# Optimization experiments

Hardware: AMD Instinct MI355X
Metric: run time of the kernel (lower is better)

Reference implementation:

```python
import jax, jax.numpy as jnp
import numpy as np

N = 50000      # num_nodes
E = 800000     # num_edges
D_IN = 128
D_HID = 128
D_EMB = 128
G = 4          # num_gcns
BN_EPS = 1e-5


def setup_inputs() -> dict:
    key = jax.random.key(0)
    ks = jax.random.split(key, 8)
    x = jax.random.normal(ks[0], (N, D_IN), dtype=jnp.float32)
    edge_index = jax.random.randint(ks[1], (2, E), 0, N, dtype=jnp.int64)
    # per-GCN params, stacked on leading G axis
    W1 = jax.random.normal(ks[2], (G, D_IN, D_HID), dtype=jnp.float32) / np.sqrt(D_IN)
    b1 = jnp.zeros((G, D_HID), dtype=jnp.float32)
    W2 = jax.random.normal(ks[3], (G, D_HID, D_EMB), dtype=jnp.float32) / np.sqrt(D_HID)
    b2 = jnp.zeros((G, D_EMB), dtype=jnp.float32)
    gamma1 = jnp.ones((G, D_HID), dtype=jnp.float32)
    beta1 = jnp.zeros((G, D_HID), dtype=jnp.float32)
    gamma2 = jnp.ones((G, D_EMB), dtype=jnp.float32)
    beta2 = jnp.zeros((G, D_EMB), dtype=jnp.float32)
    alpha = jnp.asarray(0.25, dtype=jnp.float32)  # PReLU (single shared param)
    mix_embed = jnp.full((N, G), 1.0 / G, dtype=jnp.float32)
    return {"x": x, "edge_index": edge_index, "W1": W1, "b1": b1, "W2": W2,
            "b2": b2, "gamma1": gamma1, "beta1": beta1, "gamma2": gamma2,
            "beta2": beta2, "alpha": alpha, "mix_embed": mix_embed}


def _gcn_norm(edge_index, num_nodes):
    # PyG GCNConv: add self-loops, symmetric normalization D^-1/2 (A+I) D^-1/2
    row, col = edge_index[0], edge_index[1]
    loop = jnp.arange(num_nodes, dtype=edge_index.dtype)
    row = jnp.concatenate([row, loop])
    col = jnp.concatenate([col, loop])
    w = jnp.ones(row.shape[0], dtype=jnp.float32)
    deg = jax.ops.segment_sum(w, col, num_segments=num_nodes)
    dinv = jnp.where(deg > 0, deg ** -0.5, 0.0)
    norm = dinv[row] * w * dinv[col]
    return row, col, norm


def _propagate(h, row, col, norm, num_nodes):
    # gather from source, scale by edge norm, scatter-add to target
    msg = h[row] * norm[:, None]
    return jax.ops.segment_sum(msg, col, num_segments=num_nodes)


def _batchnorm(z, gamma, beta):
    mu = jnp.mean(z, axis=0)
    var = jnp.mean((z - mu) ** 2, axis=0)  # biased, as torch BN training mode
    return (z - mu) * jax.lax.rsqrt(var + BN_EPS) * gamma + beta


def _prelu(z, alpha):
    return jnp.where(z > 0, z, alpha * z)


def reference(x, edge_index, W1, b1, W2, b2, gamma1, beta1, gamma2, beta2, alpha, mix_embed):
    num_nodes = x.shape[0]
    row, col, norm = _gcn_norm(edge_index, num_nodes)
    mix = jax.nn.softmax(mix_embed, axis=-1)  # [N, G]
    out = jnp.zeros((num_nodes, D_EMB), dtype=x.dtype)
    for g in range(G):  # small fixed number of mixture components
        h = x @ W1[g]
        z = _propagate(h, row, col, norm, num_nodes) + b1[g]
        z = _prelu(_batchnorm(z, gamma1[g], beta1[g]), alpha)
        h = z @ W2[g]
        z = _propagate(h, row, col, norm, num_nodes) + b2[g]
        z = _prelu(_batchnorm(z, gamma2[g], beta2[g]), alpha)
        out = out + mix[:, g:g + 1] * z
    return out
```

## Files before the change

### kernel.cpp

```cpp
#include <hip/hip_runtime.h>
#include <stdint.h>

static constexpr float EPS = 1e-5f;
static constexpr int XB = 64;

typedef __attribute__((ext_vector_type(8))) short bfrag;
typedef __attribute__((ext_vector_type(4))) float ffrag;

__device__ __forceinline__ float bf2f(unsigned short u){
  union { unsigned int i; float f; } v; v.i = ((unsigned int)u) << 16; return v.f;
}
__device__ __forceinline__ unsigned short f2bf(float f){
  union { float f; unsigned int i; } v; v.f = f;
  unsigned int x = v.i;
  x += 0x7fffu + ((x >> 16) & 1u);
  return (unsigned short)(x >> 16);
}
__device__ __forceinline__ float lo16(unsigned int v){ return bf2f((unsigned short)(v & 0xffffu)); }
__device__ __forceinline__ float hi16(unsigned int v){ return bf2f((unsigned short)(v >> 16)); }
__device__ __forceinline__ unsigned int pack2(float a, float b){
  return ((unsigned int)f2bf(b) << 16) | (unsigned int)f2bf(a);
}

__global__ __launch_bounds__(256) void k_deg(const int* __restrict__ col, int* __restrict__ indeg,
                                             int N, int E, int dbl,
                                             const float* __restrict__ W1, const float* __restrict__ W2,
                                             unsigned short* __restrict__ Wt1, unsigned short* __restrict__ Wt2){
  int b = blockIdx.x;
  if (b < dbl){
    int e0 = (b * 256 + threadIdx.x) * 2;
    if (e0 < E){
      if (e0 + 1 < E){
        int2 cc = *(const int2*)&col[e0];
        unsigned c0 = (unsigned)cc.x, c1 = (unsigned)cc.y;
        if (c0 < (unsigned)N) atomicAdd(&indeg[c0], 1);
        if (c1 < (unsigned)N) atomicAdd(&indeg[c1], 1);
      } else {
        unsigned c0 = (unsigned)col[e0];
        if (c0 < (unsigned)N) atomicAdd(&indeg[c0], 1);
      }
    }
  } else {
    int idx = (b - dbl) * 256 + threadIdx.x;
    const float* W = W1; unsigned short* Wt = Wt1;
    if (idx >= 65536){ idx -= 65536; W = W2; Wt = Wt2; }
    int c = idx >> 7, k = idx & 127;
    int g = c >> 7, j = c & 127;
    Wt[(size_t)c * 128 + k] = f2bf(W[(size_t)g*16384 + k*128 + j]);
  }
}

__global__ void k_alloc(const int* __restrict__ indeg, int* __restrict__ ctr,
                        int* __restrict__ offs, int* __restrict__ cursor,
                        float* __restrict__ dinv, int N){
  int tid = blockIdx.x * 256 + threadIdx.x;
  int lane = threadIdx.x & 63;
  int v = (tid < N) ? indeg[tid] : 0;
  int incl = v;
  #pragma unroll
  for (int d = 1; d < 64; d <<= 1){
    int u = __shfl_up(incl, d);
    if (lane >= d) incl += u;
  }
  int base = 0;
  if (lane == 63) base = atomicAdd(ctr, incl);
  base = __shfl(base, 63);
  if (tid < N){
    int o = base + incl - v;
    offs[tid] = o; cursor[tid] = o;
    dinv[tid] = rsqrtf((float)(v + 1));
  }
}

__global__ __launch_bounds__(256) void k_scatter(const int* __restrict__ row, const int* __restrict__ col,
                                                 int* __restrict__ cursor, int* __restrict__ csr,
                                                 int N, int E, int sbl,
                                                 const float* __restrict__ x, const float* __restrict__ dinv,
                                                 unsigned short* __restrict__ xs, int total4x){
  int b = blockIdx.x;
  if (b < sbl){
    int e0 = (b * 256 + threadIdx.x) * 2;
    #pragma unroll
    for (int q = 0; q < 2; q++){
      int e = e0 + q;
      if (e < E){
        unsigned c = (unsigned)col[e];
        if (c < (unsigned)N){
          int p = atomicAdd(&cursor[c], 1);
          unsigned r = (unsigned)row[e];
          csr[p] = (r < (unsigned)N) ? (int)r : 0;
        }
      }
    }
  } else {
    int idx = (b - sbl) * 256 + threadIdx.x;
    int stride = (gridDim.x - sbl) * 256;
    for (; idx < total4x; idx += stride){
      int i = idx >> 5;
      float di = dinv[i];
      float4 v = ((const float4*)x)[idx];
      ushort4 o;
      o.x = f2bf(di * v.x); o.y = f2bf(di * v.y);
      o.z = f2bf(di * v.z); o.w = f2bf(di * v.w);
      ((ushort4*)xs)[idx] = o;
    }
  }
}

__global__ __launch_bounds__(256) void k_prop_x(const unsigned int* __restrict__ xs2,
                                               const int* __restrict__ csr,
                                               const int* __restrict__ offs, const int* __restrict__ indeg,
                                               const float* __restrict__ dinv,
                                               unsigned int* __restrict__ s2, int N){
  int i = blockIdx.x * 4 + (threadIdx.x >> 6);
  if (i >= N) return;
  int c2 = threadIdx.x & 63;
  unsigned int sv = xs2[(size_t)i*64 + c2];
  float ax = lo16(sv), ay = hi16(sv);
  int e = offs[i], end = e + indeg[i];
  for (; e + 8 <= end; e += 8){
    int r0 = csr[e], r1 = csr[e+1], r2 = csr[e+2], r3 = csr[e+3];
    int r4 = csr[e+4], r5 = csr[e+5], r6 = csr[e+6], r7 = csr[e+7];
    unsigned int v0 = xs2[(size_t)r0*64 + c2], v1 = xs2[(size_t)r1*64 + c2];
    unsigned int v2 = xs2[(size_t)r2*64 + c2], v3 = xs2[(size_t)r3*64 + c2];
    unsigned int v4 = xs2[(size_t)r4*64 + c2], v5 = xs2[(size_t)r5*64 + c2];
    unsigned int v6 = xs2[(size_t)r6*64 + c2], v7 = xs2[(size_t)r7*64 + c2];
    ax += lo16(v0)+lo16(v1)+lo16(v2)+lo16(v3)+lo16(v4)+lo16(v5)+lo16(v6)+lo16(v7);
    ay += hi16(v0)+hi16(v1)+hi16(v2)+hi16(v3)+hi16(v4)+hi16(v5)+hi16(v6)+hi16(v7);
  }
  for (; e < end; e++){
    unsigned int v = xs2[(size_t)csr[e]*64 + c2];
    ax += lo16(v); ay += hi16(v);
  }
  float di = dinv[i];
  s2[(size_t)i*64 + c2] = pack2(di * ax, di * ay);
}

__global__ __launch_bounds__(256) void k_gram(const unsigned short* __restrict__ in,
                                              int rstride, int coff128,
                                              float* __restrict__ Gpart, float* __restrict__ msumbase,
                                              int N){
  int gy = blockIdx.y;
  const unsigned short* src = in + gy * coff128;
  float* Gp = Gpart + ((size_t)gy * XB + blockIdx.x) * 16384;
  float* msum = msumbase + gy * 128;

  __shared__ unsigned short st[128 * 40];
  __shared__ float colsum[128];

  int t = threadIdx.x;
  int wv = t >> 6, lane = t & 63, l16 = lane & 15, quad = lane >> 4;
  if (t < 128) colsum[t] = 0.f;

  int sn = t & 31, scb = t >> 5;

  ffrag acc[2][8];
  #pragma unroll
  for (int a = 0; a < 2; a++)
    #pragma unroll
    for (int b = 0; b < 8; b++) acc[a][b] = (ffrag){0.f,0.f,0.f,0.f};

  float cs[16];
  #pragma unroll
  for (int j = 0; j < 16; j++) cs[j] = 0.f;

  for (int c0 = blockIdx.x * 32; c0 < N; c0 += gridDim.x * 32){
    __syncthreads();
    int n = c0 + sn;
    ushort4 u0, u1, u2, u3;
    if (n < N){
      const ushort4* p = (const ushort4*)(src + (size_t)n * rstride + scb * 16);
      u0 = p[0]; u1 = p[1]; u2 = p[2]; u3 = p[3];
    } else {
      u0 = u1 = u2 = u3 = (ushort4){0,0,0,0};
    }
    unsigned short vals[16] = {u0.x,u0.y,u0.z,u0.w, u1.x,u1.y,u1.z,u1.w,
                               u2.x,u2.y,u2.z,u2.w, u3.x,u3.y,u3.z,u3.w};
    #pragma unroll
    for (int j = 0; j < 16; j++){
      st[(scb * 16 + j) * 40 + sn] = vals[j];
      cs[j] += bf2f(vals[j]);
    }
    __syncthreads();
    #pragma unroll
    for (int ta = 0; ta < 2; ta++){
      int ra = wv * 2 + ta;
      bfrag af = *(const bfrag*)&st[(ra * 16 + l16) * 40 + quad * 8];
      #pragma unroll
      for (int tb = 0; tb < 8; tb++){
        bfrag bf = *(const bfrag*)&st[(tb * 16 + l16) * 40 + quad * 8];
        acc[ta][tb] = __builtin_amdgcn_mfma_f32_16x16x32_bf16(af, bf, acc[ta][tb], 0, 0, 0);
      }
    }
  }
  #pragma unroll
  for (int j = 0; j < 16; j++) atomicAdd(&colsum[scb * 16 + j], cs[j]);
  __syncthreads();
  if (t < 128) atomicAdd(&msum[t], colsum[t]);
  #pragma unroll
  for (int ta = 0; ta < 2; ta++){
    #pragma unroll
    for (int tb = 0; tb < 8; tb++){
      int row0 = wv * 32 + ta * 16 + quad * 4;
      int colg = tb * 16 + l16;
      #pragma unroll
      for (int r = 0; r < 4; r++)
        Gp[(size_t)(row0 + r) * 128 + colg] = acc[ta][tb][r];
    }
  }
}

__global__ __launch_bounds__(256) void k_gred(const float* __restrict__ Gpart, float* __restrict__ G){
  int i = blockIdx.x * 256 + threadIdx.x;
  int grp = blockIdx.y;
  const float* src = Gpart + (size_t)grp * XB * 16384;
  float s = 0.f;
  #pragma unroll 4
  for (int xb = 0; xb < XB; xb++) s += src[(size_t)xb * 16384 + i];
  G[(size_t)grp * 16384 + i] = s;
}

__global__ __launch_bounds__(64) void k_bnfit(const float* __restrict__ W,
                                              const float* __restrict__ gamma, const float* __restrict__ beta,
                                              const float* __restrict__ Gbase, int gmul,
                                              const float* __restrict__ msumbase, int mmul,
                                              float* __restrict__ scale, float* __restrict__ shiftF,
                                              float invN){
  int c = blockIdx.x;
  int g = c >> 7, j = c & 127;
  const float* Wc = W + (size_t)g * 16384 + j;
  const float* G  = Gbase + (size_t)g * gmul;
  const float* mv = msumbase + g * mmul;
  __shared__ float wl[128];
  __shared__ float ml[128];
  int t = threadIdx.x;
  for (int k = t; k < 128; k += 64){ wl[k] = Wc[(size_t)k * 128]; ml[k] = mv[k] * invN; }
  __syncthreads();
  float quad = 0.f, dm = 0.f;
  #pragma unroll
  for (int kk = 0; kk < 2; kk++){
    int k = t + kk * 64;
    float wk = wl[k];
    dm += ml[k] * wk;
    const float* Gr = G + (size_t)k * 128;
    float p = 0.f;
    for (int jj = 0; jj < 128; jj += 4){
      float4 gg = *(const float4*)(Gr + jj);
      float4 ww = *(const float4*)(wl + jj);
      p += gg.x*ww.x + gg.y*ww.y + gg.z*ww.z + gg.w*ww.w;
    }
    quad += wk * p;
  }
  for (int o = 32; o > 0; o >>= 1){
    quad += __shfl_down(quad, o);
    dm   += __shfl_down(dm, o);
  }
  if (t == 0){
    float var = quad * invN - dm * dm;
    float sc = gamma[c] * rsqrtf(var + EPS);
    scale[c] = sc;
    shiftF[c] = beta[c] - dm * sc;
  }
}

__global__ __launch_bounds__(256) void k_mm1f(const unsigned short* __restrict__ in,
                                              const unsigned short* __restrict__ Wt,
                                              const float* __restrict__ scale, const float* __restrict__ shiftF,
                                              const float* __restrict__ alpha_p, const float* __restrict__ dinv,
                                              unsigned short* __restrict__ h, int N){
  float alpha = alpha_p[0];
  int wave = threadIdx.x >> 6, lane = threadIdx.x & 63;
  int l16 = lane & 15, quad = lane >> 4;
  int node = blockIdx.x * 16 + l16;
  int nc = node < N ? node : N - 1;
  int colbase0 = wave * 128;
  float di = dinv[nc];

  const unsigned short* inrow = in + (size_t)nc * 128 + quad * 8;
  bfrag b0 = *(const bfrag*)(inrow);
  bfrag b1 = *(const bfrag*)(inrow + 32);
  bfrag b2 = *(const bfrag*)(inrow + 64);
  bfrag b3 = *(const bfrag*)(inrow + 96);

  #pragma unroll
  for (int ct = 0; ct < 8; ct++){
    int colbase = colbase0 + ct * 16;
    const unsigned short* wrow = Wt + (size_t)(colbase + l16) * 128 + quad * 8;
    bfrag a0 = *(const bfrag*)(wrow);
    bfrag a1 = *(const bfrag*)(wrow + 32);
    bfrag a2 = *(const bfrag*)(wrow + 64);
    bfrag a3 = *(const bfrag*)(wrow + 96);
    ffrag acc = {0.f, 0.f, 0.f, 0.f};
    acc = __builtin_amdgcn_mfma_f32_16x16x32_bf16(a0, b0, acc, 0, 0, 0);
    acc = __builtin_amdgcn_mfma_f32_16x16x32_bf16(a1, b1, acc, 0, 0, 0);
    acc = __builtin_amdgcn_mfma_f32_16x16x32_bf16(a2, b2, acc, 0, 0, 0);
    acc = __builtin_amdgcn_mfma_f32_16x16x32_bf16(a3, b3, acc, 0, 0, 0);
    int cb = colbase + quad * 4;
    float4 sc = *(const float4*)(scale + cb);
    float4 sh = *(const float4*)(shiftF + cb);
    float v0 = acc[0]*sc.x + sh.x; v0 = v0 > 0.f ? v0 : alpha*v0;
    float v1 = acc[1]*sc.y + sh.y; v1 = v1 > 0.f ? v1 : alpha*v1;
    float v2 = acc[2]*sc.z + sh.z; v2 = v2 > 0.f ? v2 : alpha*v2;
    float v3 = acc[3]*sc.w + sh.w; v3 = v3 > 0.f ? v3 : alpha*v3;
    uint2 o;
    o.x = pack2(di*v0, di*v1);
    o.y = pack2(di*v2, di*v3);
    if (node < N)
      *(uint2*)(h + (size_t)node * 512 + cb) = o;
  }
}

__global__ __launch_bounds__(256) void k_prop_h(const unsigned int* __restrict__ h2,
                                                const int* __restrict__ csr,
                                                const int* __restrict__ offs, const int* __restrict__ indeg,
                                                const float* __restrict__ dinv,
                                                unsigned int* __restrict__ t2, int N){
  int B = blockIdx.x;
  int s = B & 3;
  int i = (B >> 2) * 4 + (threadIdx.x >> 6);
  if (i >= N) return;
  int c2 = s * 64 + (threadIdx.x & 63);
  unsigned int sv = h2[(size_t)i*256 + c2];
  float ax = lo16(sv), ay = hi16(sv);
  int e = offs[i], end = e + indeg[i];
  for (; e + 16 <= end; e += 16){
    int r[16];
    #pragma unroll
    for (int j = 0; j < 16; j++) r[j] = csr[e + j];
    unsigned int v[16];
    #pragma unroll
    for (int j = 0; j < 16; j++) v[j] = h2[(size_t)r[j]*256 + c2];
    #pragma unroll
    for (int j = 0; j < 16; j++){ ax += lo16(v[j]); ay += hi16(v[j]); }
  }
  for (; e + 4 <= end; e += 4){
    int r0 = csr[e], r1 = csr[e+1], r2 = csr[e+2], r3 = csr[e+3];
    unsigned int v0 = h2[(size_t)r0*256 + c2], v1 = h2[(size_t)r1*256 + c2];
    unsigned int v2 = h2[(size_t)r2*256 + c2], v3 = h2[(size_t)r3*256 + c2];
    ax += lo16(v0)+lo16(v1)+lo16(v2)+lo16(v3);
    ay += hi16(v0)+hi16(v1)+hi16(v2)+hi16(v3);
  }
  for (; e < end; e++){
    unsigned int v = h2[(size_t)csr[e]*256 + c2];
    ax += lo16(v); ay += hi16(v);
  }
  float di = dinv[i];
  t2[(size_t)i*256 + c2] = pack2(di * ax, di * ay);
}

__global__ __launch_bounds__(256) void k_mm2f(const unsigned short* __restrict__ t,
                                              const unsigned short* __restrict__ Wt,
                                              const float* __restrict__ scale, const float* __restrict__ shiftF,
                                              const float* __restrict__ alpha_p, const float* __restrict__ mixe,
                                              float* __restrict__ out, int N){
  __shared__ float red[4][16][132];
  float alpha = alpha_p[0];
  int wave = threadIdx.x >> 6, lane = threadIdx.x & 63;
  int l16 = lane & 15, quad = lane >> 4;
  int node = blockIdx.x * 16 + l16;
  int nc = node < N ? node : N - 1;

  float4 me = ((const float4*)mixe)[nc];
  float mx = fmaxf(fmaxf(me.x, me.y), fmaxf(me.z, me.w));
  float e0 = __expf(me.x - mx), e1 = __expf(me.y - mx), e2 = __expf(me.z - mx), e3 = __expf(me.w - mx);
  float inv = 1.f / (e0 + e1 + e2 + e3);
  float wvx = ((wave == 0) ? e0 : (wave == 1) ? e1 : (wave == 2) ? e2 : e3) * inv;

  const unsigned short* inrow = t + (size_t)nc * 512 + wave * 128 + quad * 8;
  bfrag b0 = *(const bfrag*)(inrow);
  bfrag b1 = *(const bfrag*)(inrow + 32);
  bfrag b2 = *(const bfrag*)(inrow + 64);
  bfrag b3 = *(const bfrag*)(inrow + 96);

  #pragma unroll
  for (int ct = 0; ct < 8; ct++){
    int c512 = wave * 128 + ct * 16;
    const unsigned short* wrow = Wt + (size_t)(c512 + l16) * 128 + quad * 8;
    bfrag a0 = *(const bfrag*)(wrow);
    bfrag a1 = *(const bfrag*)(wrow + 32);
    bfrag a2 = *(const bfrag*)(wrow + 64);
    bfrag a3 = *(const bfrag*)(wrow + 96);
    ffrag acc = {0.f, 0.f, 0.f, 0.f};
    acc = __builtin_amdgcn_mfma_f32_16x16x32_bf16(a0, b0, acc, 0, 0, 0);
    acc = __builtin_amdgcn_mfma_f32_16x16x32_bf16(a1, b1, acc, 0, 0, 0);
    acc = __builtin_amdgcn_mfma_f32_16x16x32_bf16(a2, b2, acc, 0, 0, 0);
    acc = __builtin_amdgcn_mfma_f32_16x16x32_bf16(a3, b3, acc, 0, 0, 0);
    int cb = c512 + quad * 4;
    float4 sc = *(const float4*)(scale + cb);
    float4 sh = *(const float4*)(shiftF + cb);
    float v0 = acc[0]*sc.x + sh.x; v0 = v0 > 0.f ? v0 : alpha*v0;
    float v1 = acc[1]*sc.y + sh.y; v1 = v1 > 0.f ? v1 : alpha*v1;
    float v2 = acc[2]*sc.z + sh.z; v2 = v2 > 0.f ? v2 : alpha*v2;
    float v3 = acc[3]*sc.w + sh.w; v3 = v3 > 0.f ? v3 : alpha*v3;
    int j = ct * 16 + quad * 4;
    float4 wr = {wvx*v0, wvx*v1, wvx*v2, wvx*v3};
    *(float4*)&red[wave][l16][j] = wr;
  }
  __syncthreads();
  int tt = threadIdx.x;
  int nn = tt >> 4, j0 = (tt & 15) * 8;
  int gnode = blockIdx.x * 16 + nn;
  if (gnode < N){
    float4 r0 = {0,0,0,0}, r1 = {0,0,0,0};
    #pragma unroll
    for (int w = 0; w < 4; w++){
      float4 p0 = *(const float4*)&red[w][nn][j0];
      float4 p1 = *(const float4*)&red[w][nn][j0 + 4];
      r0.x += p0.x; r0.y += p0.y; r0.z += p0.z; r0.w += p0.w;
      r1.x += p1.x; r1.y += p1.y; r1.z += p1.z; r1.w += p1.w;
    }
    float* op = out + (size_t)gnode * 128 + j0;
    *(float4*)(op) = r0;
    *(float4*)(op + 4) = r1;
  }
}

extern "C" void kernel_launch(void* const* d_in, const int* in_sizes, int n_in,
                              void* d_out, int out_size, void* d_ws, size_t ws_size,
                              hipStream_t stream) {
  const float* x      = (const float*)d_in[0];
  const int*   ei     = (const int*)d_in[1];
  const float* W1     = (const float*)d_in[2];
  const float* W2     = (const float*)d_in[4];
  const float* gamma1 = (const float*)d_in[6];
  const float* beta1  = (const float*)d_in[7];
  const float* gamma2 = (const float*)d_in[8];
  const float* beta2  = (const float*)d_in[9];
  const float* alpha  = (const float*)d_in[10];
  const float* mixe   = (const float*)d_in[11];
  float* out = (float*)d_out;

  const int N = in_sizes[0] / 128;
  const int E = in_sizes[1] / 2;
  const int* rowv = ei;
  const int* colv = ei + E;

  char* w = (char*)d_ws;
  size_t off = 0;
  auto take = [&](size_t bytes) -> void* {
    void* p = w + off;
    off = (off + bytes + 255) & ~(size_t)255;
    return p;
  };
  size_t zbeg = off;
  int*   indeg  = (int*)take((size_t)N * 4);
  int*   ctr    = (int*)take(256);
  float* m1     = (float*)take(512);
  float* m2     = (float*)take(2048);
  size_t zend = off;
  float* G1     = (float*)take(65536);
  float* G2     = (float*)take(262144);
  float* Gpart  = (float*)take((size_t)4 * XB * 16384 * 4);
  int*   cursor = (int*)take((size_t)N * 4);
  int*   offs   = (int*)take((size_t)N * 4);
  float* dinv   = (float*)take((size_t)N * 4);
  float* scale1 = (float*)take(2048);
  float* shift1 = (float*)take(2048);
  float* scale2 = (float*)take(2048);
  float* shift2 = (float*)take(2048);
  int*   csr    = (int*)take((size_t)E * 4);
  unsigned short* Wt1 = (unsigned short*)take(512 * 128 * 2);
  unsigned short* Wt2 = (unsigned short*)take(512 * 128 * 2);
  unsigned short* xs = (unsigned short*)take((size_t)N * 128 * 2);
  unsigned short* sb = (unsigned short*)take((size_t)N * 128 * 2);
  unsigned short* h  = (unsigned short*)take((size_t)N * 512 * 2);
  unsigned short* tb = (unsigned short*)take((size_t)N * 512 * 2);

  hipMemsetAsync((char*)d_ws + zbeg, 0, zend - zbeg, stream);

  int nb  = (N + 255) / 256;
  int dbl = (E + 511) / 512;
  float invN = 1.0f / (float)N;

  k_deg<<<dbl + 512, 256, 0, stream>>>(colv, indeg, N, E, dbl, W1, W2, Wt1, Wt2);
  k_alloc<<<nb, 256, 0, stream>>>(indeg, ctr, offs, cursor, dinv, N);
  k_scatter<<<dbl + 1024, 256, 0, stream>>>(rowv, colv, cursor, csr, N, E, dbl, x, dinv, xs, N * 32);

  k_prop_x<<<(N + 3) / 4, 256, 0, stream>>>((const unsigned int*)xs, csr, offs, indeg, dinv, (unsigned int*)sb, N);

  k_gram<<<dim3(XB, 1), 256, 0, stream>>>(sb, 128, 0, Gpart, m1, N);
  k_gred<<<dim3(64, 1), 256, 0, stream>>>(Gpart, G1);
  k_bnfit<<<512, 64, 0, stream>>>(W1, gamma1, beta1, G1, 0, m1, 0, scale1, shift1, invN);
  k_mm1f<<<(N + 15) / 16, 256, 0, stream>>>(sb, Wt1, scale1, shift1, alpha, dinv, h, N);

  k_prop_h<<<((N + 3) / 4) * 4, 256, 0, stream>>>((const unsigned int*)h, csr, offs, indeg, dinv, (unsigned int*)tb, N);

  k_gram<<<dim3(XB, 4), 256, 0, stream>>>(tb, 512, 128, Gpart, m2, N);
  k_gred<<<dim3(64, 4), 256, 0, stream>>>(Gpart, G2);
  k_bnfit<<<512, 64, 0, stream>>>(W2, gamma2, beta2, G2, 16384, m2, 128, scale2, shift2, invN);
  k_mm2f<<<(N + 15) / 16, 256, 0, stream>>>(tb, Wt2, scale2, shift2, alpha, mixe, out, N);
}
```

Baseline: 568.7 us.

## Fuse graph-build and BN-fit stages into persistent kernels with grid barriers

Merges degree counting, offset allocation and CSR scatter into one 512-block persistent kernel separated by atomic grid barriers. It also merges the Gram, reduction and BN-fit stages into a single kernel per layer. The goal is to cut launch count and inter-kernel gaps. Separately, it widens the k_prop_x gather unroll to 16 and makes k_mm1f handle 32 nodes per block so weight fragments are reused. The grid barriers assume every block is co-resident on the device, and spinning blocks plus less parallelism in the fused stages may cost time.

```diff
diff --git a/kernel.cpp b/kernel.cpp
--- a/kernel.cpp
+++ b/kernel.cpp
@@ -22,64 +22,73 @@
   return ((unsigned int)f2bf(b) << 16) | (unsigned int)f2bf(a);
 }
 
-__global__ __launch_bounds__(256) void k_deg(const int* __restrict__ col, int* __restrict__ indeg,
-                                             int N, int E, int dbl,
-                                             const float* __restrict__ W1, const float* __restrict__ W2,
-                                             unsigned short* __restrict__ Wt1, unsigned short* __restrict__ Wt2){
-  int b = blockIdx.x;
-  if (b < dbl){
-    int e0 = (b * 256 + threadIdx.x) * 2;
-    if (e0 < E){
-      if (e0 + 1 < E){
-        int2 cc = *(const int2*)&col[e0];
-        unsigned c0 = (unsigned)cc.x, c1 = (unsigned)cc.y;
-        if (c0 < (unsigned)N) atomicAdd(&indeg[c0], 1);
-        if (c1 < (unsigned)N) atomicAdd(&indeg[c1], 1);
-      } else {
-        unsigned c0 = (unsigned)col[e0];
-        if (c0 < (unsigned)N) atomicAdd(&indeg[c0], 1);
+__device__ __forceinline__ void gbar(int* cnt, int target){
+  __threadfence();
+  __syncthreads();
+  if (threadIdx.x == 0){
+    __hip_atomic_fetch_add(cnt, 1, __ATOMIC_ACQ_REL, __HIP_MEMORY_SCOPE_AGENT);
+    while (__hip_atomic_load(cnt, __ATOMIC_ACQUIRE, __HIP_MEMORY_SCOPE_AGENT) < target){
+      __builtin_amdgcn_s_sleep(8);
+    }
+  }
+  __syncthreads();
+}
+
+__global__ __launch_bounds__(256) void k_graph(const int* __restrict__ row, const int* __restrict__ col,
+                                               int N, int E,
+                                               int* __restrict__ indeg, int* __restrict__ ctr,
+                                               int* __restrict__ offs, int* __restrict__ cursor,
+                                               float* __restrict__ dinv, int* __restrict__ csr,
+                                               const float* __restrict__ x, unsigned short* __restrict__ xs,
+                                               const float* __restrict__ W1, const float* __restrict__ W2,
+                                               unsigned short* __restrict__ Wt1, unsigned short* __restrict__ Wt2,
+                                               int* __restrict__ bars){
+  int bid = blockIdx.x;
+  int gid = bid * 256 + threadIdx.x;
+  int gstride = gridDim.x * 256;
+  int target = gridDim.x;
+
+  for (int e0 = gid * 2; e0 < E; e0 += gstride * 2){
+    if (e0 + 1 < E){
+      int2 cc = *(const int2*)&col[e0];
+      unsigned c0 = (unsigned)cc.x, c1 = (unsigned)cc.y;
+      if (c0 < (unsigned)N) atomicAdd(&indeg[c0], 1);
+      if (c1 < (unsigned)N) atomicAdd(&indeg[c1], 1);
+    } else {
+      unsigned c0 = (unsigned)col[e0];
+      if (c0 < (unsigned)N) atomicAdd(&indeg[c0], 1);
+    }
+  }
+  for (int idx = gid; idx < 131072; idx += gstride){
+    int i2 = idx; const float* W = W1; unsigned short* Wt = Wt1;
+    if (i2 >= 65536){ i2 -= 65536; W = W2; Wt = Wt2; }
+    int c = i2 >> 7, k = i2 & 127;
+    Wt[(size_t)c * 128 + k] = f2bf(W[(size_t)(c >> 7) * 16384 + k * 128 + (c & 127)]);
+  }
+  gbar(&bars[0], target);
+
+  {
+    int wv = threadIdx.x >> 6, lane = threadIdx.x & 63;
+    int nwaves = gridDim.x * 4;
+    for (int wb = bid * 4 + wv; wb * 64 < N; wb += nwaves){
+      int i = wb * 64 + lane;
+      int v = (i < N) ? indeg[i] : 0;
+      int incl = v;
+      #pragma unroll
+      for (int d = 1; d < 64; d <<= 1){ int u = __shfl_up(incl, d); if (lane >= d) incl += u; }
+      int base = 0;
+      if (lane == 63) base = atomicAdd(ctr, incl);
+      base = __shfl(base, 63);
+      if (i < N){
+        int o = base + incl - v;
+        offs[i] = o; cursor[i] = o;
+        dinv[i] = rsqrtf((float)(v + 1));
       }
     }
-  } else {
-    int idx = (b - dbl) * 256 + threadIdx.x;
-    const float* W = W1; unsigned short* Wt = Wt1;
-    if (idx >= 65536){ idx -= 65536; W = W2; Wt = Wt2; }
-    int c = idx >> 7, k = idx & 127;
-    int g = c >> 7, j = c & 127;
-    Wt[(size_t)c * 128 + k] = f2bf(W[(size_t)g*16384 + k*128 + j]);
-  }
-}
-
-__global__ void k_alloc(const int* __restrict__ indeg, int* __restrict__ ctr,
-                        int* __restrict__ offs, int* __restrict__ cursor,
-                        float* __restrict__ dinv, int N){
-  int tid = blockIdx.x * 256 + threadIdx.x;
-  int lane = threadIdx.x & 63;
-  int v = (tid < N) ? indeg[tid] : 0;
-  int incl = v;
-  #pragma unroll
-  for (int d = 1; d < 64; d <<= 1){
-    int u = __shfl_up(incl, d);
-    if (lane >= d) incl += u;
-  }
-  int base = 0;
-  if (lane == 63) base = atomicAdd(ctr, incl);
-  base = __shfl(base, 63);
-  if (tid < N){
-    int o = base + incl - v;
-    offs[tid] = o; cursor[tid] = o;
-    dinv[tid] = rsqrtf((float)(v + 1));
-  }
-}
-
-__global__ __launch_bounds__(256) void k_scatter(const int* __restrict__ row, const int* __restrict__ col,
-                                                 int* __restrict__ cursor, int* __restrict__ csr,
-                                                 int N, int E, int sbl,
-                                                 const float* __restrict__ x, const float* __restrict__ dinv,
-                                                 unsigned short* __restrict__ xs, int total4x){
-  int b = blockIdx.x;
-  if (b < sbl){
-    int e0 = (b * 256 + threadIdx.x) * 2;
+  }
+  gbar(&bars[1], target);
+
+  for (int e0 = gid * 2; e0 < E; e0 += gstride * 2){
     #pragma unroll
     for (int q = 0; q < 2; q++){
       int e = e0 + q;
@@ -92,18 +101,16 @@
         }
       }
     }
-  } else {
-    int idx = (b - sbl) * 256 + threadIdx.x;
-    int stride = (gridDim.x - sbl) * 256;
-    for (; idx < total4x; idx += stride){
-      int i = idx >> 5;
-      float di = dinv[i];
-      float4 v = ((const float4*)x)[idx];
-      ushort4 o;
-      o.x = f2bf(di * v.x); o.y = f2bf(di * v.y);
-      o.z = f2bf(di * v.z); o.w = f2bf(di * v.w);
-      ((ushort4*)xs)[idx] = o;
-    }
+  }
+  int total4x = N * 32;
+  for (int idx = gid; idx < total4x; idx += gstride){
+    int i = idx >> 5;
+    float di = dinv[i];
+    float4 v = ((const float4*)x)[idx];
+    ushort4 o;
+    o.x = f2bf(di * v.x); o.y = f2bf(di * v.y);
+    o.z = f2bf(di * v.z); o.w = f2bf(di * v.w);
+    ((ushort4*)xs)[idx] = o;
   }
 }
 
@@ -118,15 +125,22 @@
   unsigned int sv = xs2[(size_t)i*64 + c2];
   float ax = lo16(sv), ay = hi16(sv);
   int e = offs[i], end = e + indeg[i];
-  for (; e + 8 <= end; e += 8){
+  for (; e + 16 <= end; e += 16){
+    int r[16];
+    #pragma unroll
+    for (int j = 0; j < 16; j++) r[j] = csr[e + j];
+    unsigned int v[16];
+    #pragma unroll
+    for (int j = 0; j < 16; j++) v[j] = xs2[(size_t)r[j]*64 + c2];
+    #pragma unroll
+    for (int j = 0; j < 16; j++){ ax += lo16(v[j]); ay += hi16(v[j]); }
+  }
+  for (; e + 4 <= end; e += 4){
     int r0 = csr[e], r1 = csr[e+1], r2 = csr[e+2], r3 = csr[e+3];
-    int r4 = csr[e+4], r5 = csr[e+5], r6 = csr[e+6], r7 = csr[e+7];
     unsigned int v0 = xs2[(size_t)r0*64 + c2], v1 = xs2[(size_t)r1*64 + c2];
     unsigned int v2 = xs2[(size_t)r2*64 + c2], v3 = xs2[(size_t)r3*64 + c2];
-    unsigned int v4 = xs2[(size_t)r4*64 + c2], v5 = xs2[(size_t)r5*64 + c2];
-    unsigned int v6 = xs2[(size_t)r6*64 + c2], v7 = xs2[(size_t)r7*64 + c2];
-    ax += lo16(v0)+lo16(v1)+lo16(v2)+lo16(v3)+lo16(v4)+lo16(v5)+lo16(v6)+lo16(v7);
-    ay += hi16(v0)+hi16(v1)+hi16(v2)+hi16(v3)+hi16(v4)+hi16(v5)+hi16(v6)+hi16(v7);
+    ax += lo16(v0)+lo16(v1)+lo16(v2)+lo16(v3);
+    ay += hi16(v0)+hi16(v1)+hi16(v2)+hi16(v3);
   }
   for (; e < end; e++){
     unsigned int v = xs2[(size_t)csr[e]*64 + c2];
@@ -136,22 +150,27 @@
   s2[(size_t)i*64 + c2] = pack2(di * ax, di * ay);
 }
 
-__global__ __launch_bounds__(256) void k_gram(const unsigned short* __restrict__ in,
-                                              int rstride, int coff128,
-                                              float* __restrict__ Gpart, float* __restrict__ msumbase,
-                                              int N){
+__global__ __launch_bounds__(256) void k_gramfit(const unsigned short* __restrict__ in,
+                                                 int rstride, int coff128,
+                                                 float* __restrict__ Gpart, float* __restrict__ msum,
+                                                 float* __restrict__ G,
+                                                 const float* __restrict__ W,
+                                                 const float* __restrict__ gamma, const float* __restrict__ beta,
+                                                 float* __restrict__ scale, float* __restrict__ shiftF,
+                                                 float invN, int N, int gmul, int mmul,
+                                                 int* __restrict__ bars){
+  __shared__ unsigned short st[128 * 40];
+  __shared__ float colsum[128];
+  __shared__ float wl[4][132], ml[4][132];
+
   int gy = blockIdx.y;
   const unsigned short* src = in + gy * coff128;
   float* Gp = Gpart + ((size_t)gy * XB + blockIdx.x) * 16384;
-  float* msum = msumbase + gy * 128;
-
-  __shared__ unsigned short st[128 * 40];
-  __shared__ float colsum[128];
+  float* ms = msum + gy * mmul;
 
   int t = threadIdx.x;
   int wv = t >> 6, lane = t & 63, l16 = lane & 15, quad = lane >> 4;
   if (t < 128) colsum[t] = 0.f;
-
   int sn = t & 31, scb = t >> 5;
 
   ffrag acc[2][8];
@@ -159,7 +178,6 @@
   for (int a = 0; a < 2; a++)
     #pragma unroll
     for (int b = 0; b < 8; b++) acc[a][b] = (ffrag){0.f,0.f,0.f,0.f};
-
   float cs[16];
   #pragma unroll
   for (int j = 0; j < 16; j++) cs[j] = 0.f;
@@ -196,7 +214,7 @@
   #pragma unroll
   for (int j = 0; j < 16; j++) atomicAdd(&colsum[scb * 16 + j], cs[j]);
   __syncthreads();
-  if (t < 128) atomicAdd(&msum[t], colsum[t]);
+  if (t < 128) atomicAdd(&ms[t], colsum[t]);
   #pragma unroll
   for (int ta = 0; ta < 2; ta++){
     #pragma unroll
@@ -208,58 +226,54 @@
         Gp[(size_t)(row0 + r) * 128 + colg] = acc[ta][tb][r];
     }
   }
-}
-
-__global__ __launch_bounds__(256) void k_gred(const float* __restrict__ Gpart, float* __restrict__ G){
-  int i = blockIdx.x * 256 + threadIdx.x;
-  int grp = blockIdx.y;
-  const float* src = Gpart + (size_t)grp * XB * 16384;
-  float s = 0.f;
-  #pragma unroll 4
-  for (int xb = 0; xb < XB; xb++) s += src[(size_t)xb * 16384 + i];
-  G[(size_t)grp * 16384 + i] = s;
-}
-
-__global__ __launch_bounds__(64) void k_bnfit(const float* __restrict__ W,
-                                              const float* __restrict__ gamma, const float* __restrict__ beta,
-                                              const float* __restrict__ Gbase, int gmul,
-                                              const float* __restrict__ msumbase, int mmul,
-                                              float* __restrict__ scale, float* __restrict__ shiftF,
-                                              float invN){
-  int c = blockIdx.x;
-  int g = c >> 7, j = c & 127;
-  const float* Wc = W + (size_t)g * 16384 + j;
-  const float* G  = Gbase + (size_t)g * gmul;
-  const float* mv = msumbase + g * mmul;
-  __shared__ float wl[128];
-  __shared__ float ml[128];
-  int t = threadIdx.x;
-  for (int k = t; k < 128; k += 64){ wl[k] = Wc[(size_t)k * 128]; ml[k] = mv[k] * invN; }
-  __syncthreads();
-  float quad = 0.f, dm = 0.f;
-  #pragma unroll
-  for (int kk = 0; kk < 2; kk++){
-    int k = t + kk * 64;
-    float wk = wl[k];
-    dm += ml[k] * wk;
-    const float* Gr = G + (size_t)k * 128;
-    float p = 0.f;
-    for (int jj = 0; jj < 128; jj += 4){
-      float4 gg = *(const float4*)(Gr + jj);
-      float4 ww = *(const float4*)(wl + jj);
-      p += gg.x*ww.x + gg.y*ww.y + gg.z*ww.z + gg.w*ww.w;
-    }
-    quad += wk * p;
-  }
-  for (int o = 32; o > 0; o >>= 1){
-    quad += __shfl_down(quad, o);
-    dm   += __shfl_down(dm, o);
-  }
-  if (t == 0){
-    float var = quad * invN - dm * dm;
-    float sc = gamma[c] * rsqrtf(var + EPS);
-    scale[c] = sc;
-    shiftF[c] = beta[c] - dm * sc;
+
+  int nblk = gridDim.x * gridDim.y;
+  gbar(&bars[0], nblk);
+
+  int gid = (blockIdx.y * gridDim.x + blockIdx.x) * 256 + t;
+  int total = gridDim.y * 16384;
+  for (int i = gid; i < total; i += nblk * 256){
+    int grp = i >> 14, e = i & 16383;
+    const float* srcp = Gpart + (size_t)grp * XB * 16384 + e;
+    float s = 0.f;
+    #pragma unroll 8
+    for (int xb = 0; xb < XB; xb++) s += srcp[(size_t)xb * 16384];
+    G[i] = s;
+  }
+  gbar(&bars[1], nblk);
+
+  int bidl = blockIdx.y * gridDim.x + blockIdx.x;
+  for (int c = bidl * 4 + wv; c < 512; c += nblk * 4){
+    int g = c >> 7, j = c & 127;
+    const float* Wc = W + (size_t)g * 16384 + j;
+    const float* Gg = G + (size_t)g * gmul;
+    const float* mv = msum + g * mmul;
+    for (int k = lane; k < 128; k += 64){ wl[wv][k] = Wc[(size_t)k * 128]; ml[wv][k] = mv[k] * invN; }
+    float quadv = 0.f, dm = 0.f;
+    #pragma unroll
+    for (int kk = 0; kk < 2; kk++){
+      int k = lane + kk * 64;
+      float wk = wl[wv][k];
+      dm += ml[wv][k] * wk;
+      const float* Gr = Gg + (size_t)k * 128;
+      float p = 0.f;
+      for (int jj = 0; jj < 128; jj += 4){
+        float4 gg = *(const float4*)(Gr + jj);
+        float4 ww = *(const float4*)(&wl[wv][jj]);
+        p += gg.x*ww.x + gg.y*ww.y + gg.z*ww.z + gg.w*ww.w;
+      }
+      quadv += wk * p;
+    }
+    for (int o = 32; o > 0; o >>= 1){
+      quadv += __shfl_down(quadv, o);
+      dm    += __shfl_down(dm, o);
+    }
+    if (lane == 0){
+      float var = quadv * invN - dm * dm;
+      float sc = gamma[c] * rsqrtf(var + EPS);
+      scale[c] = sc;
+      shiftF[c] = beta[c] - dm * sc;
+    }
   }
 }
 
@@ -271,16 +285,19 @@
   float alpha = alpha_p[0];
   int wave = threadIdx.x >> 6, lane = threadIdx.x & 63;
   int l16 = lane & 15, quad = lane >> 4;
-  int node = blockIdx.x * 16 + l16;
-  int nc = node < N ? node : N - 1;
+  int node0 = blockIdx.x * 32 + l16;
+  int node1 = node0 + 16;
+  int nc0 = node0 < N ? node0 : N - 1;
+  int nc1 = node1 < N ? node1 : N - 1;
   int colbase0 = wave * 128;
-  float di = dinv[nc];
-
-  const unsigned short* inrow = in + (size_t)nc * 128 + quad * 8;
-  bfrag b0 = *(const bfrag*)(inrow);
-  bfrag b1 = *(const bfrag*)(inrow + 32);
-  bfrag b2 = *(const bfrag*)(inrow + 64);
-  bfrag b3 = *(const bfrag*)(inrow + 96);
+  float di0 = dinv[nc0], di1 = dinv[nc1];
+
+  const unsigned short* ir0 = in + (size_t)nc0 * 128 + quad * 8;
+  const unsigned short* ir1 = in + (size_t)nc1 * 128 + quad * 8;
+  bfrag b0a = *(const bfrag*)(ir0),      b0b = *(const bfrag*)(ir1);
+  bfrag b1a = *(const bfrag*)(ir0 + 32), b1b = *(const bfrag*)(ir1 + 32);
+  bfrag b2a = *(const bfrag*)(ir0 + 64), b2b = *(const bfrag*)(ir1 + 64);
+  bfrag b3a = *(const bfrag*)(ir0 + 96), b3b = *(const bfrag*)(ir1 + 96);
 
   #pragma unroll
   for (int ct = 0; ct < 8; ct++){
@@ -290,23 +307,31 @@
     bfrag a1 = *(const bfrag*)(wrow + 32);
     bfrag a2 = *(const bfrag*)(wrow + 64);
     bfrag a3 = *(const bfrag*)(wrow + 96);
-    ffrag acc = {0.f, 0.f, 0.f, 0.f};
-    acc = __builtin_amdgcn_mfma_f32_16x16x32_bf16(a0, b0, acc, 0, 0, 0);
-    acc = __builtin_amdgcn_mfma_f32_16x16x32_bf16(a1, b1, acc, 0, 0, 0);
-    acc = __builtin_amdgcn_mfma_f32_16x16x32_bf16(a2, b2, acc, 0, 0, 0);
-    acc = __builtin_amdgcn_mfma_f32_16x16x32_bf16(a3, b3, acc, 0, 0, 0);
+    ffrag acc0 = {0.f,0.f,0.f,0.f}, acc1 = {0.f,0.f,0.f,0.f};
+    acc0 = __builtin_amdgcn_mfma_f32_16x16x32_bf16(a0, b0a, acc0, 0, 0, 0);
+    acc1 = __builtin_amdgcn_mfma_f32_16x16x32_bf16(a0, b0b, acc1, 0, 0, 0);
+    acc0 = __builtin_amdgcn_mfma_f32_16x16x32_bf16(a1, b1a, acc0, 0, 0, 0);
+    acc1 = __builtin_amdgcn_mfma_f32_16x16x32_bf16(a1, b1b, acc1, 0, 0, 0);
+    acc0 = __builtin_amdgcn_mfma_f32_16x16x32_bf16(a2, b2a, acc0, 0, 0, 0);
+    acc1 = __builtin_amdgcn_mfma_f32_16x16x32_bf16(a2, b2b, acc1, 0, 0, 0);
+    acc0 = __builtin_amdgcn_mfma_f32_16x16x32_bf16(a3, b3a, acc0, 0, 0, 0);
+    acc1 = __builtin_amdgcn_mfma_f32_16x16x32_bf16(a3, b3b, acc1, 0, 0, 0);
     int cb = colbase + quad * 4;
     float4 sc = *(const float4*)(scale + cb);
     float4 sh = *(const float4*)(shiftF + cb);
-    float v0 = acc[0]*sc.x + sh.x; v0 = v0 > 0.f ? v0 : alpha*v0;
-    float v1 = acc[1]*sc.y + sh.y; v1 = v1 > 0.f ? v1 : alpha*v1;
-    float v2 = acc[2]*sc.z + sh.z; v2 = v2 > 0.f ? v2 : alpha*v2;
-    float v3 = acc[3]*sc.w + sh.w; v3 = v3 > 0.f ? v3 : alpha*v3;
-    uint2 o;
-    o.x = pack2(di*v0, di*v1);
-    o.y = pack2(di*v2, di*v3);
-    if (node < N)
-      *(uint2*)(h + (size_t)node * 512 + cb) = o;
+    float v0 = acc0[0]*sc.x + sh.x; v0 = v0 > 0.f ? v0 : alpha*v0;
+    float v1 = acc0[1]*sc.y + sh.y; v1 = v1 > 0.f ? v1 : alpha*v1;
+    float v2 = acc0[2]*sc.z + sh.z; v2 = v2 > 0.f ? v2 : alpha*v2;
+    float v3 = acc0[3]*sc.w + sh.w; v3 = v3 > 0.f ? v3 : alpha*v3;
+    float w0 = acc1[0]*sc.x + sh.x; w0 = w0 > 0.f ? w0 : alpha*w0;
+    float w1 = acc1[1]*sc.y + sh.y; w1 = w1 > 0.f ? w1 : alpha*w1;
+    float w2 = acc1[2]*sc.z + sh.z; w2 = w2 > 0.f ? w2 : alpha*w2;
+    float w3 = acc1[3]*sc.w + sh.w; w3 = w3 > 0.f ? w3 : alpha*w3;
+    uint2 o0, o1;
+    o0.x = pack2(di0*v0, di0*v1); o0.y = pack2(di0*v2, di0*v3);
+    o1.x = pack2(di1*w0, di1*w1); o1.y = pack2(di1*w2, di1*w3);
+    if (node0 < N) *(uint2*)(h + (size_t)node0 * 512 + cb) = o0;
+    if (node1 < N) *(uint2*)(h + (size_t)node1 * 512 + cb) = o1;
   }
 }
 
@@ -445,6 +470,7 @@
   size_t zbeg = off;
   int*   indeg  = (int*)take((size_t)N * 4);
   int*   ctr    = (int*)take(256);
+  int*   bars   = (int*)take(256);
   float* m1     = (float*)take(512);
   float* m2     = (float*)take(2048);
   size_t zend = off;
@@ -468,25 +494,20 @@
 
   hipMemsetAsync((char*)d_ws + zbeg, 0, zend - zbeg, stream);
 
-  int nb  = (N + 255) / 256;
-  int dbl = (E + 511) / 512;
   float invN = 1.0f / (float)N;
 
-  k_deg<<<dbl + 512, 256, 0, stream>>>(colv, indeg, N, E, dbl, W1, W2, Wt1, Wt2);
-  k_alloc<<<nb, 256, 0, stream>>>(indeg, ctr, offs, cursor, dinv, N);
-  k_scatter<<<dbl + 1024, 256, 0, stream>>>(rowv, colv, cursor, csr, N, E, dbl, x, dinv, xs, N * 32);
+  k_graph<<<512, 256, 0, stream>>>(rowv, colv, N, E, indeg, ctr, offs, cursor, dinv, csr,
+                                   x, xs, W1, W2, Wt1, Wt2, bars);
 
   k_prop_x<<<(N + 3) / 4, 256, 0, stream>>>((const unsigned int*)xs, csr, offs, indeg, dinv, (unsigned int*)sb, N);
 
-  k_gram<<<dim3(XB, 1), 256, 0, stream>>>(sb, 128, 0, Gpart, m1, N);
-  k_gred<<<dim3(64, 1), 256, 0, stream>>>(Gpart, G1);
-  k_bnfit<<<512, 64, 0, stream>>>(W1, gamma1, beta1, G1, 0, m1, 0, scale1, shift1, invN);
-  k_mm1f<<<(N + 15) / 16, 256, 0, stream>>>(sb, Wt1, scale1, shift1, alpha, dinv, h, N);
+  k_gramfit<<<dim3(XB, 1), 256, 0, stream>>>(sb, 128, 0, Gpart, m1, G1,
+                                             W1, gamma1, beta1, scale1, shift1, invN, N, 0, 0, bars + 4);
+  k_mm1f<<<(N + 31) / 32, 256, 0, stream>>>(sb, Wt1, scale1, shift1, alpha, dinv, h, N);
 
   k_prop_h<<<((N + 3) / 4) * 4, 256, 0, stream>>>((const unsigned int*)h, csr, offs, indeg, dinv, (unsigned int*)tb, N);
 
-  k_gram<<<dim3(XB, 4), 256, 0, stream>>>(tb, 512, 128, Gpart, m2, N);
-  k_gred<<<dim3(64, 4), 256, 0, stream>>>(Gpart, G2);
-  k_bnfit<<<512, 64, 0, stream>>>(W2, gamma2, beta2, G2, 16384, m2, 128, scale2, shift2, invN);
+  k_gramfit<<<dim3(XB, 4), 256, 0, stream>>>(tb, 512, 128, Gpart, m2, G2,
+                                             W2, gamma2, beta2, scale2, shift2, invN, N, 16384, 128, bars + 8);
   k_mm2f<<<(N + 15) / 16, 256, 0, stream>>>(tb, Wt2, scale2, shift2, alpha, mixe, out, N);
 }
```

Result: slower. 783.6 us (+37.8%).

## Deepen gather unroll, process two node tiles per MFMA wave, split h-propagation into halves

Applied to the files above, without the earlier changes.

The x-propagation kernel now loads 16 neighbor indices and values at a time before accumulating, giving more memory-level parallelism on the gather. The first feature-transform kernel handles 32 nodes per block, so each weight fragment feeds two MFMA chains. The hidden-feature propagation is split into two launches, each covering half the 512-wide channel set with 128 threads per node. This keeps each pass's gather footprint smaller for cache reuse, at the cost of walking the CSR twice and higher register pressure from the larger unroll.

```diff
diff --git a/kernel.cpp b/kernel.cpp
--- a/kernel.cpp
+++ b/kernel.cpp
@@ -118,15 +118,22 @@
   unsigned int sv = xs2[(size_t)i*64 + c2];
   float ax = lo16(sv), ay = hi16(sv);
   int e = offs[i], end = e + indeg[i];
-  for (; e + 8 <= end; e += 8){
+  for (; e + 16 <= end; e += 16){
+    int r[16];
+    #pragma unroll
+    for (int j = 0; j < 16; j++) r[j] = csr[e + j];
+    unsigned int v[16];
+    #pragma unroll
+    for (int j = 0; j < 16; j++) v[j] = xs2[(size_t)r[j]*64 + c2];
+    #pragma unroll
+    for (int j = 0; j < 16; j++){ ax += lo16(v[j]); ay += hi16(v[j]); }
+  }
+  for (; e + 4 <= end; e += 4){
     int r0 = csr[e], r1 = csr[e+1], r2 = csr[e+2], r3 = csr[e+3];
-    int r4 = csr[e+4], r5 = csr[e+5], r6 = csr[e+6], r7 = csr[e+7];
     unsigned int v0 = xs2[(size_t)r0*64 + c2], v1 = xs2[(size_t)r1*64 + c2];
     unsigned int v2 = xs2[(size_t)r2*64 + c2], v3 = xs2[(size_t)r3*64 + c2];
-    unsigned int v4 = xs2[(size_t)r4*64 + c2], v5 = xs2[(size_t)r5*64 + c2];
-    unsigned int v6 = xs2[(size_t)r6*64 + c2], v7 = xs2[(size_t)r7*64 + c2];
-    ax += lo16(v0)+lo16(v1)+lo16(v2)+lo16(v3)+lo16(v4)+lo16(v5)+lo16(v6)+lo16(v7);
-    ay += hi16(v0)+hi16(v1)+hi16(v2)+hi16(v3)+hi16(v4)+hi16(v5)+hi16(v6)+hi16(v7);
+    ax += lo16(v0)+lo16(v1)+lo16(v2)+lo16(v3);
+    ay += hi16(v0)+hi16(v1)+hi16(v2)+hi16(v3);
   }
   for (; e < end; e++){
     unsigned int v = xs2[(size_t)csr[e]*64 + c2];
@@ -271,16 +278,19 @@
   float alpha = alpha_p[0];
   int wave = threadIdx.x >> 6, lane = threadIdx.x & 63;
   int l16 = lane & 15, quad = lane >> 4;
-  int node = blockIdx.x * 16 + l16;
-  int nc = node < N ? node : N - 1;
+  int node0 = blockIdx.x * 32 + l16;
+  int node1 = node0 + 16;
+  int nc0 = node0 < N ? node0 : N - 1;
+  int nc1 = node1 < N ? node1 : N - 1;
   int colbase0 = wave * 128;
-  float di = dinv[nc];
-
-  const unsigned short* inrow = in + (size_t)nc * 128 + quad * 8;
-  bfrag b0 = *(const bfrag*)(inrow);
-  bfrag b1 = *(const bfrag*)(inrow + 32);
-  bfrag b2 = *(const bfrag*)(inrow + 64);
-  bfrag b3 = *(const bfrag*)(inrow + 96);
+  float di0 = dinv[nc0], di1 = dinv[nc1];
+
+  const unsigned short* ir0 = in + (size_t)nc0 * 128 + quad * 8;
+  const unsigned short* ir1 = in + (size_t)nc1 * 128 + quad * 8;
+  bfrag b0a = *(const bfrag*)(ir0),      b0b = *(const bfrag*)(ir1);
+  bfrag b1a = *(const bfrag*)(ir0 + 32), b1b = *(const bfrag*)(ir1 + 32);
+  bfrag b2a = *(const bfrag*)(ir0 + 64), b2b = *(const bfrag*)(ir1 + 64);
+  bfrag b3a = *(const bfrag*)(ir0 + 96), b3b = *(const bfrag*)(ir1 + 96);
 
   #pragma unroll
   for (int ct = 0; ct < 8; ct++){
@@ -290,23 +300,31 @@
     bfrag a1 = *(const bfrag*)(wrow + 32);
     bfrag a2 = *(const bfrag*)(wrow + 64);
     bfrag a3 = *(const bfrag*)(wrow + 96);
-    ffrag acc = {0.f, 0.f, 0.f, 0.f};
-    acc = __builtin_amdgcn_mfma_f32_16x16x32_bf16(a0, b0, acc, 0, 0, 0);
-    acc = __builtin_amdgcn_mfma_f32_16x16x32_bf16(a1, b1, acc, 0, 0, 0);
-    acc = __builtin_amdgcn_mfma_f32_16x16x32_bf16(a2, b2, acc, 0, 0, 0);
-    acc = __builtin_amdgcn_mfma_f32_16x16x32_bf16(a3, b3, acc, 0, 0, 0);
+    ffrag acc0 = {0.f,0.f,0.f,0.f}, acc1 = {0.f,0.f,0.f,0.f};
+    acc0 = __builtin_amdgcn_mfma_f32_16x16x32_bf16(a0, b0a, acc0, 0, 0, 0);
+    acc1 = __builtin_amdgcn_mfma_f32_16x16x32_bf16(a0, b0b, acc1, 0, 0, 0);
+    acc0 = __builtin_amdgcn_mfma_f32_16x16x32_bf16(a1, b1a, acc0, 0, 0, 0);
+    acc1 = __builtin_amdgcn_mfma_f32_16x16x32_bf16(a1, b1b, acc1, 0, 0, 0);
+    acc0 = __builtin_amdgcn_mfma_f32_16x16x32_bf16(a2, b2a, acc0, 0, 0, 0);
+    acc1 = __builtin_amdgcn_mfma_f32_16x16x32_bf16(a2, b2b, acc1, 0, 0, 0);
+    acc0 = __builtin_amdgcn_mfma_f32_16x16x32_bf16(a3, b3a, acc0, 0, 0, 0);
+    acc1 = __builtin_amdgcn_mfma_f32_16x16x32_bf16(a3, b3b, acc1, 0, 0, 0);
     int cb = colbase + quad * 4;
     float4 sc = *(const float4*)(scale + cb);
     float4 sh = *(const float4*)(shiftF + cb);
-    float v0 = acc[0]*sc.x + sh.x; v0 = v0 > 0.f ? v0 : alpha*v0;
-    float v1 = acc[1]*sc.y + sh.y; v1 = v1 > 0.f ? v1 : alpha*v1;
-    float v2 = acc[2]*sc.z + sh.z; v2 = v2 > 0.f ? v2 : alpha*v2;
-    float v3 = acc[3]*sc.w + sh.w; v3 = v3 > 0.f ? v3 : alpha*v3;
-    uint2 o;
-    o.x = pack2(di*v0, di*v1);
-    o.y = pack2(di*v2, di*v3);
-    if (node < N)
-      *(uint2*)(h + (size_t)node * 512 + cb) = o;
+    float v0 = acc0[0]*sc.x + sh.x; v0 = v0 > 0.f ? v0 : alpha*v0;
+    float v1 = acc0[1]*sc.y + sh.y; v1 = v1 > 0.f ? v1 : alpha*v1;
+    float v2 = acc0[2]*sc.z + sh.z; v2 = v2 > 0.f ? v2 : alpha*v2;
+    float v3 = acc0[3]*sc.w + sh.w; v3 = v3 > 0.f ? v3 : alpha*v3;
+    float w0 = acc1[0]*sc.x + sh.x; w0 = w0 > 0.f ? w0 : alpha*w0;
+    float w1 = acc1[1]*sc.y + sh.y; w1 = w1 > 0.f ? w1 : alpha*w1;
+    float w2 = acc1[2]*sc.z + sh.z; w2 = w2 > 0.f ? w2 : alpha*w2;
+    float w3 = acc1[3]*sc.w + sh.w; w3 = w3 > 0.f ? w3 : alpha*w3;
+    uint2 o0, o1;
+    o0.x = pack2(di0*v0, di0*v1); o0.y = pack2(di0*v2, di0*v3);
+    o1.x = pack2(di1*w0, di1*w1); o1.y = pack2(di1*w2, di1*w3);
+    if (node0 < N) *(uint2*)(h + (size_t)node0 * 512 + cb) = o0;
+    if (node1 < N) *(uint2*)(h + (size_t)node1 * 512 + cb) = o1;
   }
 }
 
@@ -314,12 +332,10 @@
                                                 const int* __restrict__ csr,
                                                 const int* __restrict__ offs, const int* __restrict__ indeg,
                                                 const float* __restrict__ dinv,
-                                                unsigned int* __restrict__ t2, int N){
-  int B = blockIdx.x;
-  int s = B & 3;
-  int i = (B >> 2) * 4 + (threadIdx.x >> 6);
+                                                unsigned int* __restrict__ t2, int N, int coff){
+  int i = blockIdx.x * 2 + (threadIdx.x >> 7);
   if (i >= N) return;
-  int c2 = s * 64 + (threadIdx.x & 63);
+  int c2 = coff + (threadIdx.x & 127);
   unsigned int sv = h2[(size_t)i*256 + c2];
   float ax = lo16(sv), ay = hi16(sv);
   int e = offs[i], end = e + indeg[i];
@@ -481,9 +497,10 @@
   k_gram<<<dim3(XB, 1), 256, 0, stream>>>(sb, 128, 0, Gpart, m1, N);
   k_gred<<<dim3(64, 1), 256, 0, stream>>>(Gpart, G1);
   k_bnfit<<<512, 64, 0, stream>>>(W1, gamma1, beta1, G1, 0, m1, 0, scale1, shift1, invN);
-  k_mm1f<<<(N + 15) / 16, 256, 0, stream>>>(sb, Wt1, scale1, shift1, alpha, dinv, h, N);
-
-  k_prop_h<<<((N + 3) / 4) * 4, 256, 0, stream>>>((const unsigned int*)h, csr, offs, indeg, dinv, (unsigned int*)tb, N);
+  k_mm1f<<<(N + 31) / 32, 256, 0, stream>>>(sb, Wt1, scale1, shift1, alpha, dinv, h, N);
+
+  k_prop_h<<<(N + 1) / 2, 256, 0, stream>>>((const unsigned int*)h, csr, offs, indeg, dinv, (unsigned int*)tb, N, 0);
+  k_prop_h<<<(N + 1) / 2, 256, 0, stream>>>((const unsigned int*)h, csr, offs, indeg, dinv, (unsigned int*)tb, N, 128);
 
   k_gram<<<dim3(XB, 4), 256, 0, stream>>>(tb, 512, 128, Gpart, m2, N);
   k_gred<<<dim3(64, 4), 256, 0, stream>>>(Gpart, G2);
```

Measured after the change: 552.7 us. -2.8%, faster.
